# Kernel tuning notes

Hardware: AMD Instinct MI355X
Metric: run time of the kernel (lower is better)

The kernel has to match this reference:

```python
import jax, jax.numpy as jnp
import numpy as np

EPS = 1e-6


def setup_inputs() -> dict:
    key = jax.random.key(0)
    kq, kk, kv = jax.random.split(key, 3)
    B, H, S, D = 1, 16, 2048, 64
    q = jax.random.normal(kq, (B, H, S, D), dtype=jnp.float32)
    k = jax.random.normal(kk, (B, H, S, D), dtype=jnp.float32)
    v = jax.random.normal(kv, (B, H, S, D), dtype=jnp.float32)
    return {"q": q, "k": k, "v": v}


def reference(q, k, v):
    # Rebased linear attention: squared scaled QK score, causal mask,
    # normalized by running row-sum (not softmax).
    B, H, S, D = q.shape
    scale = D ** (-0.5)
    # [B,H,S,S] raw scores
    s = jnp.einsum("bhid,bhjd->bhij", q, k) * scale
    s2 = s * s
    causal = jnp.tril(jnp.ones((S, S), dtype=bool))  # k_idx <= q_idx
    s2 = jnp.where(causal, s2, jnp.zeros((), dtype=s2.dtype))
    z = jnp.sum(s2, axis=-1)  # [B,H,S]
    o = jnp.einsum("bhij,bhjd->bhid", s2, v)
    return o / (z[..., None] + EPS)
```

## Files before the change

### kernel.cpp

```cpp
#include <hip/hip_runtime.h>

typedef __attribute__((ext_vector_type(8))) short bf16x8;
typedef __attribute__((ext_vector_type(16))) float f32x16;

#define SLEN 2048
#define DDIM 64
#define NH 16
#define KEPS 1e-6f
#define TILE_B 16384
#define PSTR 72

__device__ __forceinline__ short f2bf(float x) {
    unsigned u = __float_as_uint(x);
    unsigned r = (u + 0x7FFFu + ((u >> 16) & 1u)) >> 16;
    return (short)r;
}
__device__ __forceinline__ unsigned cvtpk(float lo, float hi) {
    unsigned r;
    asm("v_cvt_pk_bf16_f32 %0, %1, %2" : "=v"(r) : "v"(lo), "v"(hi));
    return r;
}
__device__ __forceinline__ f32x16 mfma32x32(bf16x8 a, bf16x8 b, f32x16 c) {
    return __builtin_amdgcn_mfma_f32_32x32x16_bf16(a, b, c, 0, 0, 0);
}

__global__ void __launch_bounds__(256) prep_kernel(
    const float* __restrict__ K, const float* __restrict__ V, char* __restrict__ WS)
{
    __shared__ short vt[64 * PSTR];
    const int b  = blockIdx.x;
    const int h  = b & 15;
    const int kt = b >> 4;
    const int t  = threadIdx.x;
    const int j  = t >> 2;
    const int ks = t & 3;
    const int c16 = ks * 16;

    char* chunk = WS + ((size_t)h * 32 + kt) * TILE_B;

    {
        const float* src = K + ((size_t)h * SLEN + kt * 64 + j) * DDIM + c16;
        float4 a = ((const float4*)src)[0], bb = ((const float4*)src)[1];
        float4 c = ((const float4*)src)[2], d = ((const float4*)src)[3];
        uint4 lo = make_uint4(cvtpk(a.x,a.y), cvtpk(a.z,a.w), cvtpk(bb.x,bb.y), cvtpk(bb.z,bb.w));
        uint4 hi = make_uint4(cvtpk(c.x,c.y), cvtpk(c.z,c.w), cvtpk(d.x,d.y), cvtpk(d.z,d.w));
        *(uint4*)(chunk + ((size_t)((ks*2+0)*64 + j)) * 16) = lo;
        *(uint4*)(chunk + ((size_t)((ks*2+1)*64 + j)) * 16) = hi;
    }
    {
        const float* src = V + ((size_t)h * SLEN + kt * 64 + j) * DDIM + c16;
        float4 a = ((const float4*)src)[0], bb = ((const float4*)src)[1];
        float4 c = ((const float4*)src)[2], d = ((const float4*)src)[3];
        float f[16] = {a.x,a.y,a.z,a.w, bb.x,bb.y,bb.z,bb.w, c.x,c.y,c.z,c.w, d.x,d.y,d.z,d.w};
#pragma unroll
        for (int q = 0; q < 16; ++q)
            vt[(c16 + q) * PSTR + j] = f2bf(f[q]);
    }
    __syncthreads();
    {
        const int d  = t >> 2;
        const int jc = (t & 3) * 16;
        uint4 lo = *(const uint4*)&vt[d * PSTR + jc];
        uint4 hi = *(const uint4*)&vt[d * PSTR + jc + 8];
        char* vbase = chunk + 8192;
        *(uint4*)(vbase + (size_t)(((jc >> 4) * 2 + 0) * 64 + d) * 16) = lo;
        *(uint4*)(vbase + (size_t)(((jc >> 4) * 2 + 1) * 64 + d) * 16) = hi;
    }
}

__global__ void __launch_bounds__(256, 4) attn_main(
    const float* __restrict__ Q, const char* __restrict__ WS, float* __restrict__ O)
{
    __shared__ float red[3][64][33];

    const int bid = blockIdx.x;
    const int h   = bid & 15;
    const int u   = bid >> 4;
    const int slice = 63 - u;

    const int tid  = threadIdx.x;
    const int w    = tid >> 6;
    const int lane = tid & 63;
    const int il   = lane & 31;
    const int hi   = lane >> 5;
    const int jb   = w & 1;
    const int e    = w >> 1;

    const int g    = slice >> 1;
    const int half = slice & 1;
    const int q0   = slice * 32;

    const float* __restrict__ Qh = Q + (size_t)h * SLEN * DDIM;
    float* __restrict__ Oh = O + (size_t)h * SLEN * DDIM;
    const char* __restrict__ WSh = WS + (size_t)h * 32 * TILE_B;

    const int koff = (hi * 64 + jb * 32 + il) * 16;
    const int voff = 8192 + ((jb * 4 + hi) * 64 + il) * 16;

    bf16x8 qf[4];
#pragma unroll
    for (int ks = 0; ks < 4; ++ks) {
        const float* src = Qh + (size_t)(q0 + il) * DDIM + ks * 16 + hi * 8;
        float4 a = *reinterpret_cast<const float4*>(src);
        float4 b = *reinterpret_cast<const float4*>(src + 4);
        uint4 uq = make_uint4(cvtpk(a.x * 0.125f, a.y * 0.125f),
                              cvtpk(a.z * 0.125f, a.w * 0.125f),
                              cvtpk(b.x * 0.125f, b.y * 0.125f),
                              cvtpk(b.z * 0.125f, b.w * 0.125f));
        qf[ks] = *reinterpret_cast<bf16x8*>(&uq);
    }

    f32x16 o0, o1;
#pragma unroll
    for (int rr = 0; rr < 16; ++rr) { o0[rr] = 0.f; o1[rr] = 0.f; }
    float z = 0.f;

    const int ktend = g - ((jb > half) ? 1 : 0);

    if (e <= ktend) {
        const char* kb = WSh + (size_t)e * TILE_B + koff;
        bf16x8 kf0 = *(const bf16x8*)(kb);
        bf16x8 kf1 = *(const bf16x8*)(kb + 2048);
        bf16x8 kf2 = *(const bf16x8*)(kb + 4096);
        bf16x8 kf3 = *(const bf16x8*)(kb + 6144);
        const char* vb = WSh + (size_t)e * TILE_B + voff;
        bf16x8 v00 = *(const bf16x8*)(vb);
        bf16x8 v01 = *(const bf16x8*)(vb + 512);
        bf16x8 v10 = *(const bf16x8*)(vb + 2048);
        bf16x8 v11 = *(const bf16x8*)(vb + 2560);

        for (int kt = e; kt <= ktend; kt += 2) {
            __builtin_amdgcn_s_setprio(1);
            f32x16 sv;
#pragma unroll
            for (int rr = 0; rr < 16; ++rr) sv[rr] = 0.f;
            sv = mfma32x32(kf0, qf[0], sv);
            sv = mfma32x32(kf1, qf[1], sv);
            sv = mfma32x32(kf2, qf[2], sv);
            sv = mfma32x32(kf3, qf[3], sv);
            __builtin_amdgcn_s_setprio(0);

            if (kt + 2 <= ktend) {
                const char* nb = WSh + (size_t)(kt + 2) * TILE_B + koff;
                kf0 = *(const bf16x8*)(nb);
                kf1 = *(const bf16x8*)(nb + 2048);
                kf2 = *(const bf16x8*)(nb + 4096);
                kf3 = *(const bf16x8*)(nb + 6144);
            }

            const bool tri = (kt == g) && (jb == half);
#pragma unroll
            for (int rr = 0; rr < 16; ++rr) {
                float x = sv[rr];
                x = x * x;
                if (tri) {
                    int jl = (rr & 3) + 8 * (rr >> 2) + 4 * hi;
                    if (jl > il) x = 0.f;
                }
                sv[rr] = x;
            }
            {
                float a0 = (sv[0] + sv[1]) + (sv[2] + sv[3]);
                float a1 = (sv[4] + sv[5]) + (sv[6] + sv[7]);
                float a2 = (sv[8] + sv[9]) + (sv[10] + sv[11]);
                float a3 = (sv[12] + sv[13]) + (sv[14] + sv[15]);
                z += (a0 + a1) + (a2 + a3);
            }

            __builtin_amdgcn_s_setprio(1);
            {
                unsigned X  = cvtpk(sv[0], sv[1]);
                unsigned Xp = cvtpk(sv[2], sv[3]);
                unsigned Y  = cvtpk(sv[4], sv[5]);
                unsigned Yp = cvtpk(sv[6], sv[7]);
                asm("v_permlane32_swap_b32 %0, %1" : "+v"(X), "+v"(Y));
                asm("v_permlane32_swap_b32 %0, %1" : "+v"(Xp), "+v"(Yp));
                uint4 aw = make_uint4(X, Xp, Y, Yp);
                bf16x8 pf = *reinterpret_cast<bf16x8*>(&aw);
                o0 = mfma32x32(pf, v00, o0);
                o1 = mfma32x32(pf, v01, o1);
            }
            {
                unsigned X  = cvtpk(sv[8],  sv[9]);
                unsigned Xp = cvtpk(sv[10], sv[11]);
                unsigned Y  = cvtpk(sv[12], sv[13]);
                unsigned Yp = cvtpk(sv[14], sv[15]);
                asm("v_permlane32_swap_b32 %0, %1" : "+v"(X), "+v"(Y));
                asm("v_permlane32_swap_b32 %0, %1" : "+v"(Xp), "+v"(Yp));
                uint4 aw = make_uint4(X, Xp, Y, Yp);
                bf16x8 pf = *reinterpret_cast<bf16x8*>(&aw);
                o0 = mfma32x32(pf, v10, o0);
                o1 = mfma32x32(pf, v11, o1);
            }
            __builtin_amdgcn_s_setprio(0);

            if (kt + 2 <= ktend) {
                const char* nv = WSh + (size_t)(kt + 2) * TILE_B + voff;
                v00 = *(const bf16x8*)(nv);
                v01 = *(const bf16x8*)(nv + 512);
                v10 = *(const bf16x8*)(nv + 2048);
                v11 = *(const bf16x8*)(nv + 2560);
            }
        }
    }

    z += __shfl_xor(z, 32);
    if (w != 0) {
        float* r = &red[w - 1][lane][0];
#pragma unroll
        for (int rr = 0; rr < 16; ++rr) { r[rr] = o0[rr]; r[16 + rr] = o1[rr]; }
        r[32] = z;
    }
    __syncthreads();
    if (w == 0) {
#pragma unroll
        for (int pp = 0; pp < 3; ++pp) {
            const float* r = &red[pp][lane][0];
#pragma unroll
            for (int rr = 0; rr < 16; ++rr) { o0[rr] += r[rr]; o1[rr] += r[16 + rr]; }
            z += r[32];
        }
        const float invl = 1.f / (z + KEPS);
#pragma unroll
        for (int rr = 0; rr < 16; ++rr) {
            const int rl = (rr & 3) + 8 * (rr >> 2) + 4 * hi;
            const float inv = __shfl(invl, rl);
            Oh[(size_t)(q0 + rl) * DDIM + il]      = o0[rr] * inv;
            Oh[(size_t)(q0 + rl) * DDIM + 32 + il] = o1[rr] * inv;
        }
    }
}

__global__ void __launch_bounds__(256) attn_fp32(
    const float* __restrict__ Q, const float* __restrict__ K,
    const float* __restrict__ V, float* __restrict__ O)
{
    __shared__ float red[2][64][33];
    const int bid = blockIdx.x;
    const int h   = bid & 15;
    const int u   = bid >> 4;
    const int g   = (u < 16) ? u : (47 - u);
    const int tid  = threadIdx.x;
    const int w    = tid >> 6;
    const int lane = tid & 63;
    const int il   = lane & 31;
    const int hi   = lane >> 5;
    const int qhalf = w >> 1;
    const int jb    = w & 1;
    const int q0 = g * 64 + qhalf * 32;

    const float* Qh = Q + (size_t)h * SLEN * DDIM;
    const float* Kh = K + (size_t)h * SLEN * DDIM;
    const float* Vh = V + (size_t)h * SLEN * DDIM;
    float* Oh = O + (size_t)h * SLEN * DDIM;

    bf16x8 qf[4];
#pragma unroll
    for (int ks = 0; ks < 4; ++ks) {
        const float* src = Qh + (size_t)(q0 + il) * DDIM + ks * 16 + hi * 8;
        float4 a = *reinterpret_cast<const float4*>(src);
        float4 b = *reinterpret_cast<const float4*>(src + 4);
        uint4 uq = make_uint4(cvtpk(a.x * 0.125f, a.y * 0.125f),
                              cvtpk(a.z * 0.125f, a.w * 0.125f),
                              cvtpk(b.x * 0.125f, b.y * 0.125f),
                              cvtpk(b.z * 0.125f, b.w * 0.125f));
        qf[ks] = *reinterpret_cast<bf16x8*>(&uq);
    }
    f32x16 o0, o1;
#pragma unroll
    for (int rr = 0; rr < 16; ++rr) { o0[rr] = 0.f; o1[rr] = 0.f; }
    float z = 0.f;
    const int ktend = g - ((jb > qhalf) ? 1 : 0);

    for (int kt = 0; kt <= ktend; ++kt) {
        f32x16 sv;
#pragma unroll
        for (int rr = 0; rr < 16; ++rr) sv[rr] = 0.f;
#pragma unroll
        for (int ks = 0; ks < 4; ++ks) {
            const float* src = Kh + (size_t)(kt * 64 + jb * 32 + il) * DDIM + ks * 16 + hi * 8;
            float4 a = *reinterpret_cast<const float4*>(src);
            float4 b = *reinterpret_cast<const float4*>(src + 4);
            uint4 uk = make_uint4(cvtpk(a.x, a.y), cvtpk(a.z, a.w),
                                  cvtpk(b.x, b.y), cvtpk(b.z, b.w));
            sv = mfma32x32(*reinterpret_cast<bf16x8*>(&uk), qf[ks], sv);
        }
        const bool tri = (kt == g) && (jb == qhalf);
#pragma unroll
        for (int rr = 0; rr < 16; ++rr) {
            float x = sv[rr];
            x = x * x;
            if (tri) {
                int jl = (rr & 3) + 8 * (rr >> 2) + 4 * hi;
                if (jl > il) x = 0.f;
            }
            sv[rr] = x;
            z += x;
        }
#pragma unroll
        for (int s16 = 0; s16 < 2; ++s16) {
            unsigned X  = cvtpk(sv[8*s16+0], sv[8*s16+1]);
            unsigned Xp = cvtpk(sv[8*s16+2], sv[8*s16+3]);
            unsigned Y  = cvtpk(sv[8*s16+4], sv[8*s16+5]);
            unsigned Yp = cvtpk(sv[8*s16+6], sv[8*s16+7]);
            asm("v_permlane32_swap_b32 %0, %1" : "+v"(X), "+v"(Y));
            asm("v_permlane32_swap_b32 %0, %1" : "+v"(Xp), "+v"(Yp));
            uint4 aw = make_uint4(X, Xp, Y, Yp);
            bf16x8 pf = *reinterpret_cast<bf16x8*>(&aw);
#pragma unroll
            for (int dt = 0; dt < 2; ++dt) {
                float v8[8];
#pragma unroll
                for (int t = 0; t < 8; ++t)
                    v8[t] = Vh[(size_t)(kt * 64 + jb * 32 + s16 * 16 + hi * 8 + t) * DDIM + dt * 32 + il];
                uint4 uv = make_uint4(cvtpk(v8[0], v8[1]), cvtpk(v8[2], v8[3]),
                                      cvtpk(v8[4], v8[5]), cvtpk(v8[6], v8[7]));
                bf16x8 vf = *reinterpret_cast<bf16x8*>(&uv);
                if (dt == 0) o0 = mfma32x32(pf, vf, o0);
                else         o1 = mfma32x32(pf, vf, o1);
            }
        }
    }

    z += __shfl_xor(z, 32);
    if (jb == 1) {
        float* r = &red[qhalf][lane][0];
#pragma unroll
        for (int rr = 0; rr < 16; ++rr) { r[rr] = o0[rr]; r[16 + rr] = o1[rr]; }
        r[32] = z;
    }
    __syncthreads();
    if (jb == 0) {
        const float* r = &red[qhalf][lane][0];
#pragma unroll
        for (int rr = 0; rr < 16; ++rr) { o0[rr] += r[rr]; o1[rr] += r[16 + rr]; }
        z += r[32];
        const float invl = 1.f / (z + KEPS);
#pragma unroll
        for (int rr = 0; rr < 16; ++rr) {
            const int rl = (rr & 3) + 8 * (rr >> 2) + 4 * hi;
            const float inv = __shfl(invl, rl);
            Oh[(size_t)(q0 + rl) * DDIM + il]      = o0[rr] * inv;
            Oh[(size_t)(q0 + rl) * DDIM + 32 + il] = o1[rr] * inv;
        }
    }
}

extern "C" void kernel_launch(void* const* d_in, const int* in_sizes, int n_in,
                              void* d_out, int out_size, void* d_ws, size_t ws_size,
                              hipStream_t stream) {
    const float* q = (const float*)d_in[0];
    const float* k = (const float*)d_in[1];
    const float* v = (const float*)d_in[2];
    float* o = (float*)d_out;

    const size_t need = (size_t)NH * 32 * TILE_B;
    if (ws_size >= need) {
        char* ws = (char*)d_ws;
        hipLaunchKernelGGL(prep_kernel, dim3(NH * 32), dim3(256), 0, stream, k, v, ws);
        hipLaunchKernelGGL(attn_main, dim3(1024), dim3(256), 0, stream, q, ws, o);
    } else {
        hipLaunchKernelGGL(attn_fp32, dim3(512), dim3(256), 0, stream, q, k, v, o);
    }
}
```

Baseline: 29.12 us.

## Double-buffer K fragments two tiles ahead and drop setprio hints

Restructures the attention main loop to keep two sets of K fragment registers (A/B), unrolled by two iterations, so K loads are issued two tiles ahead of use rather than one. The s_setprio hints around MFMA sections are removed. Launch bounds drop from 4 to 3 waves per EU to make room for the extra registers. The aim is to hide global-load latency for K, at the cost of lower occupancy and higher register pressure.

```diff
diff --git a/kernel.cpp b/kernel.cpp
--- a/kernel.cpp
+++ b/kernel.cpp
@@ -68,7 +68,7 @@
     }
 }
 
-__global__ void __launch_bounds__(256, 4) attn_main(
+__global__ void __launch_bounds__(256, 3) attn_main(
     const float* __restrict__ Q, const char* __restrict__ WS, float* __restrict__ O)
 {
     __shared__ float red[3][64][33];
@@ -118,36 +118,21 @@
     const int ktend = g - ((jb > half) ? 1 : 0);
 
     if (e <= ktend) {
-        const char* kb = WSh + (size_t)e * TILE_B + koff;
-        bf16x8 kf0 = *(const bf16x8*)(kb);
-        bf16x8 kf1 = *(const bf16x8*)(kb + 2048);
-        bf16x8 kf2 = *(const bf16x8*)(kb + 4096);
-        bf16x8 kf3 = *(const bf16x8*)(kb + 6144);
-        const char* vb = WSh + (size_t)e * TILE_B + voff;
-        bf16x8 v00 = *(const bf16x8*)(vb);
-        bf16x8 v01 = *(const bf16x8*)(vb + 512);
-        bf16x8 v10 = *(const bf16x8*)(vb + 2048);
-        bf16x8 v11 = *(const bf16x8*)(vb + 2560);
-
-        for (int kt = e; kt <= ktend; kt += 2) {
-            __builtin_amdgcn_s_setprio(1);
+        bf16x8 kA0, kA1, kA2, kA3;
+        bf16x8 kB0, kB1, kB2, kB3;
+        bf16x8 v00, v01, v10, v11;
+
+        auto qkt = [&](bf16x8 k0, bf16x8 k1, bf16x8 k2, bf16x8 k3) -> f32x16 {
             f32x16 sv;
 #pragma unroll
             for (int rr = 0; rr < 16; ++rr) sv[rr] = 0.f;
-            sv = mfma32x32(kf0, qf[0], sv);
-            sv = mfma32x32(kf1, qf[1], sv);
-            sv = mfma32x32(kf2, qf[2], sv);
-            sv = mfma32x32(kf3, qf[3], sv);
-            __builtin_amdgcn_s_setprio(0);
-
-            if (kt + 2 <= ktend) {
-                const char* nb = WSh + (size_t)(kt + 2) * TILE_B + koff;
-                kf0 = *(const bf16x8*)(nb);
-                kf1 = *(const bf16x8*)(nb + 2048);
-                kf2 = *(const bf16x8*)(nb + 4096);
-                kf3 = *(const bf16x8*)(nb + 6144);
-            }
-
+            sv = mfma32x32(k0, qf[0], sv);
+            sv = mfma32x32(k1, qf[1], sv);
+            sv = mfma32x32(k2, qf[2], sv);
+            sv = mfma32x32(k3, qf[3], sv);
+            return sv;
+        };
+        auto finish = [&](f32x16 sv, int kt) {
             const bool tri = (kt == g) && (jb == half);
 #pragma unroll
             for (int rr = 0; rr < 16; ++rr) {
@@ -166,8 +151,6 @@
                 float a3 = (sv[12] + sv[13]) + (sv[14] + sv[15]);
                 z += (a0 + a1) + (a2 + a3);
             }
-
-            __builtin_amdgcn_s_setprio(1);
             {
                 unsigned X  = cvtpk(sv[0], sv[1]);
                 unsigned Xp = cvtpk(sv[2], sv[3]);
@@ -192,16 +175,37 @@
                 o0 = mfma32x32(pf, v10, o0);
                 o1 = mfma32x32(pf, v11, o1);
             }
-            __builtin_amdgcn_s_setprio(0);
-
-            if (kt + 2 <= ktend) {
-                const char* nv = WSh + (size_t)(kt + 2) * TILE_B + voff;
-                v00 = *(const bf16x8*)(nv);
-                v01 = *(const bf16x8*)(nv + 512);
-                v10 = *(const bf16x8*)(nv + 2048);
-                v11 = *(const bf16x8*)(nv + 2560);
-            }
-        }
+        };
+
+#define LOAD_KA(kt_) { const char* p_ = WSh + (size_t)(kt_) * TILE_B + koff; \
+        kA0 = *(const bf16x8*)(p_); kA1 = *(const bf16x8*)(p_ + 2048); \
+        kA2 = *(const bf16x8*)(p_ + 4096); kA3 = *(const bf16x8*)(p_ + 6144); }
+#define LOAD_KB(kt_) { const char* p_ = WSh + (size_t)(kt_) * TILE_B + koff; \
+        kB0 = *(const bf16x8*)(p_); kB1 = *(const bf16x8*)(p_ + 2048); \
+        kB2 = *(const bf16x8*)(p_ + 4096); kB3 = *(const bf16x8*)(p_ + 6144); }
+#define LOAD_V(kt_) { const char* p_ = WSh + (size_t)(kt_) * TILE_B + voff; \
+        v00 = *(const bf16x8*)(p_); v01 = *(const bf16x8*)(p_ + 512); \
+        v10 = *(const bf16x8*)(p_ + 2048); v11 = *(const bf16x8*)(p_ + 2560); }
+
+        LOAD_KA(e);
+        LOAD_KB((e + 2 <= ktend) ? e + 2 : e);
+        LOAD_V(e);
+
+        for (int kt = e; kt <= ktend; kt += 4) {
+            f32x16 sv = qkt(kA0, kA1, kA2, kA3);
+            { int kn = (kt + 4 <= ktend) ? kt + 4 : kt; LOAD_KA(kn); }
+            finish(sv, kt);
+            if (kt + 2 > ktend) break;
+            LOAD_V(kt + 2);
+
+            sv = qkt(kB0, kB1, kB2, kB3);
+            { int kn = (kt + 6 <= ktend) ? kt + 6 : kt + 2; LOAD_KB(kn); }
+            finish(sv, kt + 2);
+            { int kn = (kt + 4 <= ktend) ? kt + 4 : kt + 2; LOAD_V(kn); }
+        }
+#undef LOAD_KA
+#undef LOAD_KB
+#undef LOAD_V
     }
 
     z += __shfl_xor(z, 32);
```

Measured after the change: 29.66 us. No clear change (+1.9%).
